# Optimization experiments

Measured on AMD Instinct MI355X. Metric: run time of the kernel, lower is better.

The kernel has to match this reference:

```python
import jax, jax.numpy as jnp
import numpy as np

BETA = 0.9       # membrane decay
THR = 1.0        # snntorch Leaky default threshold
SLOPE = 25.0     # fast_sigmoid surrogate slope (forward-only here)


def _heaviside(x):
    return (x > 0).astype(x.dtype)


def setup_inputs() -> dict:
    key = jax.random.key(0)
    ks = jax.random.split(key, 4)
    B, D, H1, H2, C = 4096, 1024, 2048, 1024, 64
    x = jax.random.normal(ks[0], (B, D), jnp.float32)
    W1 = jax.random.normal(ks[1], (H1, D), jnp.float32) * 0.02
    b1 = jnp.zeros((H1,), jnp.float32)
    W2 = jax.random.normal(ks[2], (H2, H1), jnp.float32) * 0.02
    b2 = jnp.zeros((H2,), jnp.float32)
    Wo = jax.random.normal(ks[3], (C, H2), jnp.float32) * 0.02
    bo = jnp.zeros((C,), jnp.float32)
    return {"x": x, "W1": W1, "b1": b1, "W2": W2, "b2": b2,
            "Wo": Wo, "bo": bo, "num_steps": 20}


def reference(x, W1, b1, W2, b2, Wo, bo, num_steps):
    B = x.shape[0]
    mem1 = jnp.zeros((B, W1.shape[0]), x.dtype)
    mem2 = jnp.zeros((B, W2.shape[0]), x.dtype)
    spk_sum = jnp.zeros((B, W2.shape[0]), x.dtype)

    def step(carry, _):
        cur, m1, m2, ss = carry
        # Layer 1: Linear + Leaky (reset-by-subtraction, persistent mem)
        h1 = cur @ W1.T + b1                      # [B, H1]
        r1 = _heaviside(m1 - THR)                 # reset from previous mem
        m1 = BETA * m1 + h1 - r1 * THR
        s1 = _heaviside(m1 - THR)
        # Layer 2: Linear + Leaky
        h2 = s1 @ W2.T + b2                       # [B, H2]
        r2 = _heaviside(m2 - THR)
        m2 = BETA * m2 + h2 - r2 * THR
        s2 = _heaviside(m2 - THR)
        # NOTE: s2 feeds back into layer-1 Linear next step (cur = x only at t=0)
        return (s2, m1, m2, ss + s2), None

    (cur, mem1, mem2, spk_sum), _ = jax.lax.scan(
        step, (x, mem1, mem2, spk_sum), None, length=num_steps)
    return (spk_sum / num_steps) @ Wo.T + bo
```

## Files before the change

### kernel.cpp

```cpp
#include <hip/hip_runtime.h>
#include <hip/hip_bf16.h>

#define B_   4096
#define D_   1024
#define H1_  2048
#define H2_  1024
#define C_   64

typedef double d4 __attribute__((ext_vector_type(4)));

#if defined(__has_builtin)
#  if __has_builtin(__builtin_amdgcn_mfma_f64_16x16x4f64)
#    define MFMA64(A, B, C) __builtin_amdgcn_mfma_f64_16x16x4f64((A), (B), (C), 0, 0, 0)
#    define HAVE_MFMA64 1
#  elif __has_builtin(__builtin_amdgcn_mfma_f64_16x16x4_f64)
#    define MFMA64(A, B, C) __builtin_amdgcn_mfma_f64_16x16x4_f64((A), (B), (C), 0, 0, 0)
#    define HAVE_MFMA64 1
#  endif
#endif

__global__ void k_probe(int* flag) {
#if defined(HAVE_MFMA64)
    int lane = threadIdx.x & 63;
    int lr = lane & 15, lk = lane >> 4;
    double a  = (double)(5 * lr + 3 * lk + 1);
    double bb = (double)(11 * lk + 2 * lr + 2);
    d4 c = {0.0, 0.0, 0.0, 0.0};
    c = MFMA64(a, bb, c);
    int okm[4] = {1, 1, 1, 1};
#pragma unroll
    for (int j = 0; j < 4; ++j) {
        double e1 = 0, e2 = 0, e3 = 0, e4 = 0;
        for (int k = 0; k < 4; ++k) {
            e1 += (double)(5 * (4 * lk + j) + 3 * k + 1) * (double)(11 * k + 2 * lr + 2);
            e2 += (double)(5 * lr + 3 * k + 1) * (double)(11 * k + 2 * (4 * lk + j) + 2);
            e3 += (double)(5 * (lk + 4 * j) + 3 * k + 1) * (double)(11 * k + 2 * lr + 2);
            e4 += (double)(5 * lr + 3 * k + 1) * (double)(11 * k + 2 * (lk + 4 * j) + 2);
        }
        if (c[j] != e1) okm[0] = 0;
        if (c[j] != e2) okm[1] = 0;
        if (c[j] != e3) okm[2] = 0;
        if (c[j] != e4) okm[3] = 0;
    }
    int f = 0;
    for (int m = 3; m >= 0; --m) {
        unsigned long long all = __ballot(okm[m] != 0);
        if (all == ~0ULL) f = m + 1;
    }
    if (lane == 0) flag[0] = f;
#else
    if ((threadIdx.x & 63) == 0) flag[0] = 0;
#endif
}

__global__ __launch_bounds__(256) void k_transpose(const float* __restrict__ in,
                                                   float* __restrict__ out,
                                                   int R, int C) {
    __shared__ float t[32][33];
    int c0 = blockIdx.x * 32;
    int r0 = blockIdx.y * 32;
    int lx = threadIdx.x;
    int ly = threadIdx.y;
#pragma unroll
    for (int q = 0; q < 4; ++q) {
        int rr = ly + 8 * q;
        t[rr][lx] = in[(size_t)(r0 + rr) * C + (c0 + lx)];
    }
    __syncthreads();
#pragma unroll
    for (int q = 0; q < 4; ++q) {
        int cc = ly + 8 * q;
        out[(size_t)(c0 + cc) * R + (r0 + lx)] = t[lx][cc];
    }
}

#define GBM 128
#define GBN 128
#define GBK 64
#define ASZ32 8832
__device__ __forceinline__ int AIDX32(int k, int r) {
    return k * 136 + ((k >> 2) << 3) + ((k & 1) << 3) + r;
}
__global__ __launch_bounds__(512, 4) void k_gemm_mfma(const float* __restrict__ x,
                                                      const float* __restrict__ W1,
                                                      const float* __restrict__ b1,
                                                      double* __restrict__ m1out,
                                                      const int* __restrict__ flag) {
#if defined(HAVE_MFMA64)
    int fm = flag[0];
    if (fm < 1 || fm > 4) return;
    __shared__ float As[ASZ32];
    __shared__ float Bs[ASZ32];

    int tid = threadIdx.x;
    int m0 = blockIdx.x * GBM;
    int n0 = blockIdx.y * GBN;
    int w = tid >> 6, lane = tid & 63;
    int wr = w >> 2;
    int wc = w & 3;
    int lr = lane & 15, lk = lane >> 4;

    int srow = tid >> 2;
    int g    = tid & 3;
    int woff = AIDX32(4 * g, srow);

    const float* xrow = x  + (size_t)(m0 + srow) * D_;
    const float* wrow = W1 + (size_t)(n0 + srow) * D_;

    d4 acc[4][2];
#pragma unroll
    for (int i = 0; i < 4; ++i)
#pragma unroll
        for (int j = 0; j < 2; ++j) acc[i][j] = (d4){0.0, 0.0, 0.0, 0.0};

    for (int k0 = 0; k0 < D_; k0 += GBK) {
        float4 av[4], bv[4];
#pragma unroll
        for (int q = 0; q < 4; ++q) {
            av[q] = *(const float4*)&xrow[k0 + 4 * g + 16 * q];
            bv[q] = *(const float4*)&wrow[k0 + 4 * g + 16 * q];
        }
        __syncthreads();
#pragma unroll
        for (int q = 0; q < 4; ++q) {
            int o = woff + q * 2208;
            As[o +   0] = av[q].x;
            As[o + 144] = av[q].y;
            As[o + 272] = av[q].z;
            As[o + 416] = av[q].w;
            Bs[o +   0] = bv[q].x;
            Bs[o + 144] = bv[q].y;
            Bs[o + 272] = bv[q].z;
            Bs[o + 416] = bv[q].w;
        }
        __syncthreads();
#pragma unroll
        for (int kb = 0; kb < 16; ++kb) {
            int k = kb * 4 + lk;
            int abase = AIDX32(k, wr * 64 + lr);
            int bbase = AIDX32(k, wc * 32 + lr);
            double a[4], bfr[2];
#pragma unroll
            for (int i = 0; i < 4; ++i) a[i]   = (double)As[abase + 16 * i];
#pragma unroll
            for (int j = 0; j < 2; ++j) bfr[j] = (double)Bs[bbase + 16 * j];
#pragma unroll
            for (int i = 0; i < 4; ++i)
#pragma unroll
                for (int j = 0; j < 2; ++j)
                    acc[i][j] = MFMA64(a[i], bfr[j], acc[i][j]);
        }
    }

#pragma unroll
    for (int j = 0; j < 2; ++j)
#pragma unroll
        for (int i = 0; i < 4; ++i)
#pragma unroll
            for (int r = 0; r < 4; ++r) {
                int rin = (fm == 1) ? (4 * lk + r) : (fm == 2) ? lr
                        : (fm == 3) ? (lk + 4 * r) : lr;
                int cin = (fm == 1) ? lr : (fm == 2) ? (4 * lk + r)
                        : (fm == 3) ? lr : (lk + 4 * r);
                int row = m0 + wr * 64 + 16 * i + rin;
                int col = n0 + wc * 32 + 16 * j + cin;
                m1out[(size_t)row * H1_ + col] = acc[i][j][r] + (double)b1[col];
            }
#else
    (void)x; (void)W1; (void)b1; (void)m1out; (void)flag;
#endif
}

#define BM 128
#define BN 128
#define BK 8
__global__ __launch_bounds__(256) void k_gemm1(const float* __restrict__ x,
                                               const float* __restrict__ W1,
                                               const float* __restrict__ b1,
                                               double* __restrict__ m1out,
                                               const int* __restrict__ flag) {
    int fm = flag[0];
    if (fm >= 1 && fm <= 4) return;
    __shared__ double As[BK][BM + 4];
    __shared__ double Bs[BK][BN + 4];

    int tid = threadIdx.x;
    int m0 = blockIdx.x * BM;
    int n0 = blockIdx.y * BN;
    int tx = tid & 15;
    int ty = tid >> 4;
    int lr = tid >> 1;
    int lk = (tid & 1) * 4;

    double acc[8][8] = {};

    for (int k0 = 0; k0 < D_; k0 += BK) {
        float4 av = *(const float4*)&x [(size_t)(m0 + lr) * D_ + k0 + lk];
        float4 bv = *(const float4*)&W1[(size_t)(n0 + lr) * D_ + k0 + lk];
        __syncthreads();
        As[lk + 0][lr] = (double)av.x;
        As[lk + 1][lr] = (double)av.y;
        As[lk + 2][lr] = (double)av.z;
        As[lk + 3][lr] = (double)av.w;
        Bs[lk + 0][lr] = (double)bv.x;
        Bs[lk + 1][lr] = (double)bv.y;
        Bs[lk + 2][lr] = (double)bv.z;
        Bs[lk + 3][lr] = (double)bv.w;
        __syncthreads();
#pragma unroll
        for (int kk = 0; kk < BK; ++kk) {
            double a[8], b[8];
#pragma unroll
            for (int i = 0; i < 8; ++i) a[i] = As[kk][tx + 16 * i];
#pragma unroll
            for (int j = 0; j < 8; ++j) b[j] = Bs[kk][ty + 16 * j];
#pragma unroll
            for (int i = 0; i < 8; ++i)
#pragma unroll
                for (int j = 0; j < 8; ++j)
                    acc[i][j] += a[i] * b[j];
        }
    }
#pragma unroll
    for (int j = 0; j < 8; ++j) {
        double bj = (double)b1[n0 + ty + 16 * j];
#pragma unroll
        for (int i = 0; i < 8; ++i) {
            m1out[(size_t)(m0 + tx + 16 * i) * H1_ + (n0 + ty + 16 * j)] =
                acc[i][j] + bj;
        }
    }
}

__global__ __launch_bounds__(256) void k_snn(const double* __restrict__ m1_0,
                                             const float* __restrict__ b1,
                                             const float* __restrict__ W1T,
                                             const float* __restrict__ W2T,
                                             const float* __restrict__ b2,
                                             const float* __restrict__ Wo,
                                             const float* __restrict__ bo,
                                             const int* __restrict__ nsteps_p,
                                             float* __restrict__ out) {
    __shared__ __align__(16) double pjbuf[H2_];
    __shared__ __align__(16) int l2idx[H2_];
    __shared__ unsigned long long s1by[32];
    __shared__ unsigned long long s2nb[32];
    __shared__ int ncnt[2];
    __shared__ int anyb1[4], anyb2[4];

    int* l1idx = (int*)pjbuf;

    int b = blockIdx.x;
    int tid = threadIdx.x;
    int lane = tid & 63;
    int wv = tid >> 6;
    int T = nsteps_p[0];

    double m1r[8], m2r[4];
    float b1f[8], b2f[4];
    int cnt[4];

    const double* m1p = m1_0 + (size_t)b * H1_ + 8 * tid;
    {
        double2 v0 = *(const double2*)(m1p + 0);
        double2 v1 = *(const double2*)(m1p + 2);
        double2 v2 = *(const double2*)(m1p + 4);
        double2 v3 = *(const double2*)(m1p + 6);
        m1r[0] = v0.x; m1r[1] = v0.y; m1r[2] = v1.x; m1r[3] = v1.y;
        m1r[4] = v2.x; m1r[5] = v2.y; m1r[6] = v3.x; m1r[7] = v3.y;
    }
    {
        float4 f0 = *(const float4*)(b1 + 8 * tid);
        float4 f1 = *(const float4*)(b1 + 8 * tid + 4);
        b1f[0] = f0.x; b1f[1] = f0.y; b1f[2] = f0.z; b1f[3] = f0.w;
        b1f[4] = f1.x; b1f[5] = f1.y; b1f[6] = f1.z; b1f[7] = f1.w;
        float4 f2 = *(const float4*)(b2 + 4 * tid);
        b2f[0] = f2.x; b2f[1] = f2.y; b2f[2] = f2.z; b2f[3] = f2.w;
    }
#pragma unroll
    for (int q = 0; q < 4; ++q) { m2r[q] = 0.0; cnt[q] = 0; }

    int anyS2 = 0;

#define ACC2(v) { m2r[0] += (double)(v).x; m2r[1] += (double)(v).y; \
                  m2r[2] += (double)(v).z; m2r[3] += (double)(v).w; }

    for (int t = 0; t < T; ++t) {
        if (t > 0) {
#pragma unroll
            for (int q = 0; q < 8; ++q)
                m1r[q] = 0.9 * m1r[q] - (m1r[q] > 1.0 ? 1.0 : 0.0) + (double)b1f[q];
            if (anyS2) {
                int n2 = ncnt[1];
                const char* Wc = (const char*)W1T;
                size_t toff = (size_t)tid << 5;
                for (int k2 = 0; k2 < n2; ++k2) {
                    const float4* c4 = (const float4*)(Wc + l2idx[k2] + toff);
                    float4 va = c4[0];
                    float4 vb = c4[1];
                    m1r[0] += (double)va.x; m1r[1] += (double)va.y;
                    m1r[2] += (double)va.z; m1r[3] += (double)va.w;
                    m1r[4] += (double)vb.x; m1r[5] += (double)vb.y;
                    m1r[6] += (double)vb.z; m1r[7] += (double)vb.w;
                }
            }
        }
        unsigned bflag = 0;
#pragma unroll
        for (int q = 0; q < 8; ++q) bflag |= (m1r[q] > 1.0 ? 1u : 0u) << q;
        ((unsigned char*)s1by)[tid] = (unsigned char)bflag;
        {
            int wa = __any((int)bflag);
            if (lane == 0) anyb1[wv] = wa;
        }
#pragma unroll
        for (int q = 0; q < 4; ++q)
            m2r[q] = 0.9 * m2r[q] - (m2r[q] > 1.0 ? 1.0 : 0.0) + (double)b2f[q];
        {
            unsigned nib = 0;
#pragma unroll
            for (int q = 0; q < 4; ++q) nib |= (m2r[q] > 1.0 ? 1u : 0u) << q;
            ((unsigned char*)s2nb)[tid] = (unsigned char)nib;
            int wa = __any((int)nib);
            if (lane == 0) anyb2[wv] = wa;
        }
        __syncthreads();
        int any1 = anyb1[0] | anyb1[1] | anyb1[2] | anyb1[3];
        if (any1) {
            if (tid < 64) {
                unsigned long long bits = (tid < 32) ? s1by[tid] : 0ULL;
                int pc = __popcll(bits);
                int sc = pc;
#pragma unroll
                for (int d = 1; d < 64; d <<= 1) {
                    int o = __shfl_up(sc, d);
                    if (tid >= d) sc += o;
                }
                if (tid == 63) ncnt[0] = sc;
                int off = sc - pc;
                int base = tid << 6;
                while (bits) {
                    l1idx[off++] = (base + __builtin_ctzll(bits)) << 12;
                    bits &= bits - 1;
                }
            }
            __syncthreads();
            {
                int n1 = ncnt[0];
                const char* Wc = (const char*)W2T;
                size_t toff = (size_t)tid << 4;
                int k = 0;
                for (; k + 8 <= n1; k += 8) {
                    int4 oa = *(const int4*)&l1idx[k];
                    int4 ob = *(const int4*)&l1idx[k + 4];
                    float4 v0 = *(const float4*)(Wc + oa.x + toff);
                    float4 v1 = *(const float4*)(Wc + oa.y + toff);
                    float4 v2 = *(const float4*)(Wc + oa.z + toff);
                    float4 v3 = *(const float4*)(Wc + oa.w + toff);
                    float4 v4 = *(const float4*)(Wc + ob.x + toff);
                    float4 v5 = *(const float4*)(Wc + ob.y + toff);
                    float4 v6 = *(const float4*)(Wc + ob.z + toff);
                    float4 v7 = *(const float4*)(Wc + ob.w + toff);
                    ACC2(v0); ACC2(v1); ACC2(v2); ACC2(v3);
                    ACC2(v4); ACC2(v5); ACC2(v6); ACC2(v7);
                }
                for (; k < n1; ++k) {
                    float4 v = *(const float4*)(Wc + l1idx[k] + toff);
                    ACC2(v);
                }
            }
            {
                unsigned nib = 0;
#pragma unroll
                for (int q = 0; q < 4; ++q) nib |= (m2r[q] > 1.0 ? 1u : 0u) << q;
                ((unsigned char*)s2nb)[tid] = (unsigned char)nib;
                int wa = __any((int)nib);
                if (lane == 0) anyb2[wv] = wa;
            }
            __syncthreads();
        }
        anyS2 = anyb2[0] | anyb2[1] | anyb2[2] | anyb2[3];
#pragma unroll
        for (int q = 0; q < 4; ++q) cnt[q] += (m2r[q] > 1.0) ? 1 : 0;
        if (anyS2) {
            if (tid < 64) {
                unsigned long long wbits = 0ULL;
                if (tid < 16) {
                    unsigned long long w0 = s2nb[2 * tid];
                    unsigned long long w1 = s2nb[2 * tid + 1];
                    w0 &= 0x0F0F0F0F0F0F0F0FULL;
                    w0 = (w0 | (w0 >> 4)) & 0x00FF00FF00FF00FFULL;
                    w0 = (w0 | (w0 >> 8)) & 0x0000FFFF0000FFFFULL;
                    w0 = (w0 | (w0 >> 16)) & 0x00000000FFFFFFFFULL;
                    w1 &= 0x0F0F0F0F0F0F0F0FULL;
                    w1 = (w1 | (w1 >> 4)) & 0x00FF00FF00FF00FFULL;
                    w1 = (w1 | (w1 >> 8)) & 0x0000FFFF0000FFFFULL;
                    w1 = (w1 | (w1 >> 16)) & 0x00000000FFFFFFFFULL;
                    wbits = w0 | (w1 << 32);
                }
                int pc = __popcll(wbits);
                int sc = pc;
#pragma unroll
                for (int d = 1; d < 64; d <<= 1) {
                    int o = __shfl_up(sc, d);
                    if (tid >= d) sc += o;
                }
                if (tid == 63) ncnt[1] = sc;
                int off = sc - pc;
                int base = tid << 6;
                while (wbits) {
                    l2idx[off++] = (base + __builtin_ctzll(wbits)) << 13;
                    wbits &= wbits - 1;
                }
            }
            __syncthreads();
        }
    }
#undef ACC2

    __syncthreads();
#pragma unroll
    for (int q = 0; q < 4; ++q)
        pjbuf[4 * tid + q] = (double)cnt[q] / (double)T;
    {
        unsigned nib = 0;
#pragma unroll
        for (int q = 0; q < 4; ++q) nib |= (cnt[q] > 0 ? 1u : 0u) << q;
        ((unsigned char*)s2nb)[tid] = (unsigned char)nib;
    }
    __syncthreads();
    if (tid < 64) {
        unsigned long long wbits = 0ULL;
        if (tid < 16) {
            unsigned long long w0 = s2nb[2 * tid];
            unsigned long long w1 = s2nb[2 * tid + 1];
            w0 &= 0x0F0F0F0F0F0F0F0FULL;
            w0 = (w0 | (w0 >> 4)) & 0x00FF00FF00FF00FFULL;
            w0 = (w0 | (w0 >> 8)) & 0x0000FFFF0000FFFFULL;
            w0 = (w0 | (w0 >> 16)) & 0x00000000FFFFFFFFULL;
            w1 &= 0x0F0F0F0F0F0F0F0FULL;
            w1 = (w1 | (w1 >> 4)) & 0x00FF00FF00FF00FFULL;
            w1 = (w1 | (w1 >> 8)) & 0x0000FFFF0000FFFFULL;
            w1 = (w1 | (w1 >> 16)) & 0x00000000FFFFFFFFULL;
            wbits = w0 | (w1 << 32);
        }
        int pc = __popcll(wbits);
        int sc = pc;
#pragma unroll
        for (int d = 1; d < 64; d <<= 1) {
            int o = __shfl_up(sc, d);
            if (tid >= d) sc += o;
        }
        if (tid == 63) ncnt[1] = sc;
        int off = sc - pc;
        int base = tid << 6;
        while (wbits) {
            l2idx[off++] = base + __builtin_ctzll(wbits);
            wbits &= wbits - 1;
        }
    }
    __syncthreads();
    if (tid < C_) {
        int c = tid;
        int na = ncnt[1];
        const float* worow = &Wo[(size_t)c * H2_];
        double acc = 0.0;
        for (int k = 0; k < na; ++k) {
            int j = l2idx[k];
            acc += pjbuf[j] * (double)worow[j];
        }
        out[(size_t)b * C_ + c] = (float)(acc + (double)bo[c]);
    }
}

extern "C" void kernel_launch(void* const* d_in, const int* in_sizes, int n_in,
                              void* d_out, int out_size, void* d_ws, size_t ws_size,
                              hipStream_t stream) {
    const float* x  = (const float*)d_in[0];
    const float* W1 = (const float*)d_in[1];
    const float* b1 = (const float*)d_in[2];
    const float* W2 = (const float*)d_in[3];
    const float* b2 = (const float*)d_in[4];
    const float* Wo = (const float*)d_in[5];
    const float* bo = (const float*)d_in[6];
    const int* nst  = (const int*)d_in[7];
    float* out = (float*)d_out;

    size_t off_m1   = 0;
    size_t off_w1t  = off_m1 + (size_t)B_ * H1_ * 8;
    size_t off_w2t  = off_w1t + (size_t)D_ * H1_ * 4;
    size_t off_flag = off_w2t + (size_t)H1_ * H2_ * 4;
    size_t need     = off_flag + 64;
    if (ws_size < need) return;

    double* m1ws = (double*)((char*)d_ws + off_m1);
    float*  W1T  = (float*)((char*)d_ws + off_w1t);
    float*  W2T  = (float*)((char*)d_ws + off_w2t);
    int*    flag = (int*)((char*)d_ws + off_flag);

    k_probe<<<1, 64, 0, stream>>>(flag);

    k_transpose<<<dim3(D_ / 32, H1_ / 32), dim3(32, 8), 0, stream>>>(W1, W1T, H1_, D_);
    k_transpose<<<dim3(H1_ / 32, H2_ / 32), dim3(32, 8), 0, stream>>>(W2, W2T, H2_, H1_);

    k_gemm_mfma<<<dim3(B_ / GBM, H1_ / GBN), 512, 0, stream>>>(x, W1, b1, m1ws, flag);
    k_gemm1<<<dim3(B_ / BM, H1_ / BN), 256, 0, stream>>>(x, W1, b1, m1ws, flag);

    k_snn<<<B_, 256, 0, stream>>>(m1ws, b1, W1T, W2T, b2, Wo, bo, nst, out);
}
```

Before: 440.9 us.

## Add double-buffered async global-to-LDS FP64 MFMA GEMM for layer-1 input

Adds a new first-layer GEMM kernel that transposes x into workspace and streams K-major tiles of x and W1 straight into LDS with global_load_lds, double-buffering so the next tile loads while MFMA f64 runs on the current one. Tiles shrink to 128x64x32 with a higher occupancy hint. The old register-staged kernel is kept as a fallback when the builtin or extra workspace is missing. This costs an extra transpose of x and more workspace in exchange for less register staging and overlapped loads.

```diff
diff --git a/kernel.cpp b/kernel.cpp
--- a/kernel.cpp
+++ b/kernel.cpp
@@ -17,6 +17,16 @@
 #    define MFMA64(A, B, C) __builtin_amdgcn_mfma_f64_16x16x4_f64((A), (B), (C), 0, 0, 0)
 #    define HAVE_MFMA64 1
 #  endif
+#  if __has_builtin(__builtin_amdgcn_global_load_lds)
+#    define HAVE_GLL 1
+#  endif
+#endif
+
+#if defined(HAVE_GLL)
+#define GLOAD16(gsrc, ldst)                                                    \
+    __builtin_amdgcn_global_load_lds(                                          \
+        (const __attribute__((address_space(1))) unsigned int*)(const void*)(gsrc), \
+        (__attribute__((address_space(3))) unsigned int*)(void*)(ldst), 16, 0, 0)
 #endif
 
 __global__ void k_probe(int* flag) {
@@ -75,17 +85,107 @@
 }
 
 #define GBM 128
-#define GBN 128
-#define GBK 64
+#define GBN 64
+#define GBK 32
+#define ATILE (GBK * GBM)
+#define BTILE (GBK * GBN)
+__global__ __launch_bounds__(512, 6) void k_gemm_async(const float* __restrict__ xT,
+                                                       const float* __restrict__ W1T,
+                                                       const float* __restrict__ b1,
+                                                       double* __restrict__ m1out,
+                                                       const int* __restrict__ flag) {
+#if defined(HAVE_MFMA64) && defined(HAVE_GLL)
+    int fm = flag[0];
+    if (fm < 1 || fm > 4) return;
+    __shared__ float As[2][ATILE];
+    __shared__ float Bs[2][BTILE];
+
+    int tid = threadIdx.x;
+    int m0 = blockIdx.x * GBM;
+    int n0 = blockIdx.y * GBN;
+    int w = tid >> 6, lane = tid & 63;
+    int wr = w >> 1;
+    int wc = w & 1;
+    int lr = lane & 15, lk = lane >> 4;
+
+    const float* srcA0base = xT + (size_t)(4 * w + (lane >> 5)) * B_ + m0 + 4 * (lane & 31);
+    const float* srcA1base = srcA0base + 2 * B_;
+    const float* srcBbase = W1T + (size_t)(4 * w + (lane >> 4)) * H1_ + n0 + 4 * (lane & 15);
+
+    d4 acc[2][2];
+#pragma unroll
+    for (int i = 0; i < 2; ++i)
+#pragma unroll
+        for (int j = 0; j < 2; ++j) acc[i][j] = (d4){0.0, 0.0, 0.0, 0.0};
+
+    const int NT = D_ / GBK;
+
+    GLOAD16(srcA0base, &As[0][(2 * w + 0) * 256]);
+    GLOAD16(srcA1base, &As[0][(2 * w + 1) * 256]);
+    GLOAD16(srcBbase,  &Bs[0][w * 256]);
+    __syncthreads();
+
+    int cur = 0;
+    for (int t = 0; t < NT; ++t) {
+        if (t + 1 < NT) {
+            size_t koff = (size_t)(t + 1) * GBK;
+            GLOAD16(srcA0base + koff * B_,  &As[cur ^ 1][(2 * w + 0) * 256]);
+            GLOAD16(srcA1base + koff * B_,  &As[cur ^ 1][(2 * w + 1) * 256]);
+            GLOAD16(srcBbase  + koff * H1_, &Bs[cur ^ 1][w * 256]);
+        }
+        const float* Ac = As[cur];
+        const float* Bc = Bs[cur];
+#pragma unroll
+        for (int kb = 0; kb < 8; ++kb) {
+            int k = kb * 4 + lk;
+            const float* Ak = Ac + k * GBM;
+            const float* Bk = Bc + k * GBN;
+            double a[2], bfr[2];
+#pragma unroll
+            for (int i = 0; i < 2; ++i) a[i]   = (double)Ak[wr * 32 + 16 * i + lr];
+#pragma unroll
+            for (int j = 0; j < 2; ++j) bfr[j] = (double)Bk[wc * 32 + 16 * j + lr];
+#pragma unroll
+            for (int i = 0; i < 2; ++i)
+#pragma unroll
+                for (int j = 0; j < 2; ++j)
+                    acc[i][j] = MFMA64(a[i], bfr[j], acc[i][j]);
+        }
+        __syncthreads();
+        cur ^= 1;
+    }
+
+#pragma unroll
+    for (int j = 0; j < 2; ++j)
+#pragma unroll
+        for (int i = 0; i < 2; ++i)
+#pragma unroll
+            for (int r = 0; r < 4; ++r) {
+                int rin = (fm == 1) ? (4 * lk + r) : (fm == 2) ? lr
+                        : (fm == 3) ? (lk + 4 * r) : lr;
+                int cin = (fm == 1) ? lr : (fm == 2) ? (4 * lk + r)
+                        : (fm == 3) ? lr : (lk + 4 * r);
+                int row = m0 + wr * 32 + 16 * i + rin;
+                int col = n0 + wc * 32 + 16 * j + cin;
+                m1out[(size_t)row * H1_ + col] = acc[i][j][r] + (double)b1[col];
+            }
+#else
+    (void)xT; (void)W1T; (void)b1; (void)m1out; (void)flag;
+#endif
+}
+
+#define VBM 128
+#define VBN 128
+#define VBK 64
 #define ASZ32 8832
 __device__ __forceinline__ int AIDX32(int k, int r) {
     return k * 136 + ((k >> 2) << 3) + ((k & 1) << 3) + r;
 }
-__global__ __launch_bounds__(512, 4) void k_gemm_mfma(const float* __restrict__ x,
-                                                      const float* __restrict__ W1,
-                                                      const float* __restrict__ b1,
-                                                      double* __restrict__ m1out,
-                                                      const int* __restrict__ flag) {
+__global__ __launch_bounds__(512, 4) void k_gemm_v8(const float* __restrict__ x,
+                                                    const float* __restrict__ W1,
+                                                    const float* __restrict__ b1,
+                                                    double* __restrict__ m1out,
+                                                    const int* __restrict__ flag) {
 #if defined(HAVE_MFMA64)
     int fm = flag[0];
     if (fm < 1 || fm > 4) return;
@@ -93,8 +193,8 @@
     __shared__ float Bs[ASZ32];
 
     int tid = threadIdx.x;
-    int m0 = blockIdx.x * GBM;
-    int n0 = blockIdx.y * GBN;
+    int m0 = blockIdx.x * VBM;
+    int n0 = blockIdx.y * VBN;
     int w = tid >> 6, lane = tid & 63;
     int wr = w >> 2;
     int wc = w & 3;
@@ -113,7 +213,7 @@
 #pragma unroll
         for (int j = 0; j < 2; ++j) acc[i][j] = (d4){0.0, 0.0, 0.0, 0.0};
 
-    for (int k0 = 0; k0 < D_; k0 += GBK) {
+    for (int k0 = 0; k0 < D_; k0 += VBK) {
         float4 av[4], bv[4];
 #pragma unroll
         for (int q = 0; q < 4; ++q) {
@@ -151,7 +251,6 @@
                     acc[i][j] = MFMA64(a[i], bfr[j], acc[i][j]);
         }
     }
-
 #pragma unroll
     for (int j = 0; j < 2; ++j)
 #pragma unroll
@@ -492,18 +591,32 @@
     size_t off_flag = off_w2t + (size_t)H1_ * H2_ * 4;
     size_t need     = off_flag + 64;
     if (ws_size < need) return;
+    size_t off_xt   = off_flag + 64;
+    size_t need_async = off_xt + (size_t)D_ * B_ * 4;
 
     double* m1ws = (double*)((char*)d_ws + off_m1);
     float*  W1T  = (float*)((char*)d_ws + off_w1t);
     float*  W2T  = (float*)((char*)d_ws + off_w2t);
     int*    flag = (int*)((char*)d_ws + off_flag);
+    float*  xT   = (float*)((char*)d_ws + off_xt);
+
+#if defined(HAVE_GLL)
+    bool use_async = (ws_size >= need_async);
+#else
+    bool use_async = false;
+#endif
 
     k_probe<<<1, 64, 0, stream>>>(flag);
 
     k_transpose<<<dim3(D_ / 32, H1_ / 32), dim3(32, 8), 0, stream>>>(W1, W1T, H1_, D_);
     k_transpose<<<dim3(H1_ / 32, H2_ / 32), dim3(32, 8), 0, stream>>>(W2, W2T, H2_, H1_);
 
-    k_gemm_mfma<<<dim3(B_ / GBM, H1_ / GBN), 512, 0, stream>>>(x, W1, b1, m1ws, flag);
+    if (use_async) {
+        k_transpose<<<dim3(D_ / 32, B_ / 32), dim3(32, 8), 0, stream>>>(x, xT, B_, D_);
+        k_gemm_async<<<dim3(B_ / GBM, H1_ / GBN), 512, 0, stream>>>(xT, W1T, b1, m1ws, flag);
+    } else {
+        k_gemm_v8<<<dim3(B_ / VBM, H1_ / VBN), 512, 0, stream>>>(x, W1, b1, m1ws, flag);
+    }
     k_gemm1<<<dim3(B_ / BM, H1_ / BN), 256, 0, stream>>>(x, W1, b1, m1ws, flag);
 
     k_snn<<<B_, 256, 0, stream>>>(m1ws, b1, W1T, W2T, b2, Wo, bo, nst, out);
```

Measured after the change: 440.8 us. About the same (-0.0%).
